# Optimization experiments

Hardware: AMD Instinct MI355X
Metric: run time of the kernel (lower is better)

## Reference

```python
import jax, jax.numpy as jnp
import numpy as np

DIM = 128
HEADS = 4
GH, GW = 14, 14
N = GH * GW            # 196
POS_DIM = (DIM // 4) // 4  # 8, per DynamicPosBias(dim//4): pos_dim = (dim//4)//4
B_ = 1024
NW = 64
EPS = 1e-5


def _make_bias_tables():
    # biases: all relative (dh, dw) offsets, shape ((2*GH-1)*(2*GW-1), 2)
    h = np.arange(1 - GH, GH)
    w = np.arange(1 - GW, GW)
    bh, bw = np.meshgrid(h, w, indexing='ij')
    biases = np.stack([bh.ravel(), bw.ravel()], axis=1).astype(np.float32)
    # relative_position_index: (N, N) int
    ch, cw = np.meshgrid(np.arange(GH), np.arange(GW), indexing='ij')
    coords = np.stack([ch.ravel(), cw.ravel()])          # (2, N)
    rel = coords[:, :, None] - coords[:, None, :]        # (2, N, N)
    rel = rel.transpose(1, 2, 0).copy()
    rel[:, :, 0] += GH - 1
    rel[:, :, 1] += GW - 1
    rel[:, :, 0] *= 2 * GW - 1
    idx = rel.sum(-1).astype(np.int32)                   # (N, N)
    return jnp.asarray(biases), jnp.asarray(idx)


def setup_inputs() -> dict:
    key = jax.random.key(0)
    ks = jax.random.split(key, 12)
    s_in = 1.0 / np.sqrt(DIM)
    s_p = 1.0 / np.sqrt(POS_DIM)
    biases, rel_idx = _make_bias_tables()
    return {
        'x': jax.random.normal(ks[0], (B_, N, DIM), jnp.float32),
        'mask': jnp.zeros((NW, N, N), jnp.float32),
        # qkv / proj (stored as (in, out), i.e. torch weight transposed)
        'qkv_w': jax.random.normal(ks[1], (DIM, 3 * DIM), jnp.float32) * s_in,
        'qkv_b': jnp.zeros((3 * DIM,), jnp.float32),
        'proj_w': jax.random.normal(ks[2], (DIM, DIM), jnp.float32) * s_in,
        'proj_b': jnp.zeros((DIM,), jnp.float32),
        # DynamicPosBias params
        'pos_proj_w': jax.random.normal(ks[3], (2, POS_DIM), jnp.float32) * 0.5,
        'pos_proj_b': jnp.zeros((POS_DIM,), jnp.float32),
        'ln1_w': jnp.ones((POS_DIM,), jnp.float32), 'ln1_b': jnp.zeros((POS_DIM,), jnp.float32),
        'fc1_w': jax.random.normal(ks[4], (POS_DIM, POS_DIM), jnp.float32) * s_p,
        'fc1_b': jnp.zeros((POS_DIM,), jnp.float32),
        'ln2_w': jnp.ones((POS_DIM,), jnp.float32), 'ln2_b': jnp.zeros((POS_DIM,), jnp.float32),
        'fc2_w': jax.random.normal(ks[5], (POS_DIM, POS_DIM), jnp.float32) * s_p,
        'fc2_b': jnp.zeros((POS_DIM,), jnp.float32),
        'ln3_w': jnp.ones((POS_DIM,), jnp.float32), 'ln3_b': jnp.zeros((POS_DIM,), jnp.float32),
        'fc3_w': jax.random.normal(ks[6], (POS_DIM, HEADS), jnp.float32) * s_p,
        'fc3_b': jnp.zeros((HEADS,), jnp.float32),
        'biases': biases,       # ((2GH-1)*(2GW-1), 2) float32
        'rel_idx': rel_idx,     # (N, N) int32
    }


def _ln(x, w, b):
    mu = x.mean(-1, keepdims=True)
    var = ((x - mu) ** 2).mean(-1, keepdims=True)
    return (x - mu) * jax.lax.rsqrt(var + EPS) * w + b


def reference(x, mask, qkv_w, qkv_b, proj_w, proj_b,
              pos_proj_w, pos_proj_b,
              ln1_w, ln1_b, fc1_w, fc1_b,
              ln2_w, ln2_b, fc2_w, fc2_b,
              ln3_w, ln3_b, fc3_w, fc3_b,
              biases, rel_idx):
    B, n, C = x.shape
    hd = C // HEADS
    scale = hd ** -0.5

    qkv = (x @ qkv_w + qkv_b).reshape(B, n, 3, HEADS, hd)
    q, k, v = jnp.moveaxis(qkv, 2, 0)          # each (B, n, H, hd)
    q = q * scale
    attn = jnp.einsum('bqhd,bkhd->bhqk', q, k)  # (B, H, n, n)

    # DynamicPosBias (residual=False): pos3(pos2(pos1(pos_proj(biases))))
    p = biases @ pos_proj_w + pos_proj_b
    p = jax.nn.relu(_ln(p, ln1_w, ln1_b)) @ fc1_w + fc1_b
    p = jax.nn.relu(_ln(p, ln2_w, ln2_b)) @ fc2_w + fc2_b
    p = jax.nn.relu(_ln(p, ln3_w, ln3_b)) @ fc3_w + fc3_b   # (L, H)
    rpb = p[rel_idx]                            # (n, n, H) gather
    attn = attn + jnp.transpose(rpb, (2, 0, 1))[None]

    nW = mask.shape[0]
    attn = attn.reshape(B // nW, nW, HEADS, n, n) + mask[None, :, None]
    attn = jax.nn.softmax(attn.reshape(B, HEADS, n, n), axis=-1)

    out = jnp.einsum('bhqk,bkhd->bqhd', attn, v).reshape(B, n, C)
    return out @ proj_w + proj_b
```

## Files before the change

### kernel.cpp

```cpp
#include <hip/hip_runtime.h>
#include <stdint.h>

#define N_TOK 196
#define DIM   128
#define HEADS 4
#define NWIN  64
#define SCALE 0.17677669529663687f
#define LOG2E 1.4426950408889634f
#define PS_LD 232

typedef __bf16 bf16x8 __attribute__((ext_vector_type(8)));
typedef float  f32x4  __attribute__((ext_vector_type(4)));

__device__ __forceinline__ unsigned short f2bf(float f) {
  unsigned r;
  asm("v_cvt_pk_bf16_f32 %0, %1, %2" : "=v"(r) : "v"(f), "v"(f));
  return (unsigned short)r;
}
__device__ __forceinline__ unsigned pack2(float a, float b) {
  unsigned r;
  asm("v_cvt_pk_bf16_f32 %0, %1, %2" : "=v"(r) : "v"(a), "v"(b));
  return r;
}
__device__ __forceinline__ float fexp2(float x) {
  float r;
  asm("v_exp_f32 %0, %1" : "=v"(r) : "v"(x));
  return r;
}

__global__ void prep_kernel(
    const float* __restrict__ qkv_w, const float* __restrict__ proj_w,
    const float* __restrict__ biases,
    const float* __restrict__ pos_proj_w, const float* __restrict__ pos_proj_b,
    const float* __restrict__ ln1_w, const float* __restrict__ ln1_b,
    const float* __restrict__ fc1_w, const float* __restrict__ fc1_b,
    const float* __restrict__ ln2_w, const float* __restrict__ ln2_b,
    const float* __restrict__ fc2_w, const float* __restrict__ fc2_b,
    const float* __restrict__ ln3_w, const float* __restrict__ ln3_b,
    const float* __restrict__ fc3_w, const float* __restrict__ fc3_b,
    unsigned short* __restrict__ wqkv_t, unsigned short* __restrict__ wproj_t,
    float* __restrict__ ptab)
{
  const int tid = threadIdx.x, blk = blockIdx.x;
  if (blk < 3) {
    int r = blk * 256 + tid;
    if (r < 729) {
      float v[8], t[8];
      float b0 = biases[2*r], b1 = biases[2*r+1];
      for (int j = 0; j < 8; ++j)
        v[j] = b0 * pos_proj_w[j] + b1 * pos_proj_w[8+j] + pos_proj_b[j];
      const float* lws[3] = {ln1_w, ln2_w, ln3_w};
      const float* lbs[3] = {ln1_b, ln2_b, ln3_b};
      const float* fws[3] = {fc1_w, fc2_w, fc3_w};
      const float* fbs[3] = {fc1_b, fc2_b, fc3_b};
      for (int L = 0; L < 3; ++L) {
        float mu = 0.f;  for (int j=0;j<8;++j) mu += v[j];  mu *= 0.125f;
        float var = 0.f; for (int j=0;j<8;++j){ float d=v[j]-mu; var+=d*d; } var *= 0.125f;
        float rs = rsqrtf(var + 1e-5f);
        for (int j=0;j<8;++j){ float u=(v[j]-mu)*rs*lws[L][j]+lbs[L][j]; t[j]=fmaxf(u,0.f); }
        int nout = (L==2) ? 4 : 8;
        for (int o=0;o<nout;++o){ float s=fbs[L][o]; for (int j=0;j<8;++j) s += t[j]*fws[L][j*nout+o]; v[o]=s; }
      }
      for (int hh=0; hh<4; ++hh) ptab[r*4+hh] = v[hh];
    }
  } else if (blk < 7) {
    for (int i = (blk-3)*256 + tid; i < 384*128; i += 1024) {
      int col = i >> 7, k = i & 127;
      wqkv_t[i] = f2bf(qkv_w[k*384 + col]);
    }
  } else {
    for (int i = tid; i < 128*128; i += 256) {
      int col = i >> 7, k = i & 127;
      wproj_t[i] = f2bf(proj_w[k*128 + col]);
    }
  }
}

__global__ void comb_kernel(const int* __restrict__ rel_idx,
                            const float* __restrict__ ptab,
                            const float* __restrict__ mask,
                            float* __restrict__ combT)
{
  int blk = blockIdx.x;
  int w = blk / 196, k = blk - w*196;
  int q = threadIdx.x;
  if (q < N_TOK) {
    int idx = rel_idx[q*N_TOK + k];
    float mv = mask[((size_t)w*N_TOK + q)*N_TOK + k];
    #pragma unroll
    for (int h = 0; h < 4; ++h)
      combT[((size_t)(w*4 + h)*196 + k)*196 + q] = (ptab[idx*4 + h] + mv) * LOG2E;
  }
}

__launch_bounds__(256, 2)
__global__ void qkv_kernel(const float* __restrict__ x,
                           const float* __restrict__ qkv_b,
                           const unsigned short* __restrict__ wqkv_t,
                           unsigned short* __restrict__ q_g,
                           unsigned short* __restrict__ k_g,
                           unsigned short* __restrict__ vt_g)
{
  const int tid = threadIdx.x;
  const int wave = tid >> 6, lane = tid & 63, lr = lane & 15, lg = lane >> 4;
  const int b = blockIdx.x;
  const float* xb = x + (size_t)b * (N_TOK*DIM);

  bf16x8 wf[6][4];
  float  bq[6];
  f32x4  bv[6];
  #pragma unroll
  for (int i = 0; i < 6; ++i) {
    const int g = wave*6 + i;
    #pragma unroll
    for (int kc = 0; kc < 4; ++kc)
      wf[i][kc] = *(const bf16x8*)(wqkv_t + (g*16 + lr)*128 + kc*32 + lg*8);
    if (g < 16) {
      bq[i] = qkv_b[g*16 + lr];
      bv[i] = (f32x4){0.f,0.f,0.f,0.f};
    } else {
      bq[i] = 0.f;
      #pragma unroll
      for (int r = 0; r < 4; ++r) bv[i][r] = qkv_b[g*16 + lg*4 + r];
    }
  }

  auto load_xf = [&](int rt, bf16x8* xf) {
    const int arow = rt*16 + lr;
    #pragma unroll
    for (int kc = 0; kc < 4; ++kc) {
      union { unsigned u[4]; bf16x8 v; } c;
      if (arow < N_TOK) {
        float4 p0 = *(const float4*)(xb + arow*DIM + kc*32 + lg*8);
        float4 p1 = *(const float4*)(xb + arow*DIM + kc*32 + lg*8 + 4);
        c.u[0] = pack2(p0.x, p0.y); c.u[1] = pack2(p0.z, p0.w);
        c.u[2] = pack2(p1.x, p1.y); c.u[3] = pack2(p1.z, p1.w);
      } else {
        c.u[0] = c.u[1] = c.u[2] = c.u[3] = 0u;
      }
      xf[kc] = c.v;
    }
  };

  bf16x8 xf[4], xfn[4];
  load_xf(0, xf);
  for (int rt = 0; rt < 13; ++rt) {
    if (rt < 12) load_xf(rt + 1, xfn);
    #pragma unroll
    for (int i = 0; i < 6; ++i) {
      const int g = wave*6 + i;
      f32x4 acc = {0.f,0.f,0.f,0.f};
      if (g >= 16) {
        #pragma unroll
        for (int kc = 0; kc < 4; ++kc)
          acc = __builtin_amdgcn_mfma_f32_16x16x32_bf16(wf[i][kc], xf[kc], acc, 0, 0, 0);
        const int dt = g - 16;
        #pragma unroll
        for (int r = 0; r < 4; ++r)
          vt_g[((size_t)b*128 + dt*16 + lg*4 + r)*224 + rt*16 + lr] =
              f2bf(acc[r] + bv[i][r]);
      } else {
        #pragma unroll
        for (int kc = 0; kc < 4; ++kc)
          acc = __builtin_amdgcn_mfma_f32_16x16x32_bf16(xf[kc], wf[i][kc], acc, 0, 0, 0);
        const int cs = (g < 8) ? g*16 : (g-8)*16;
        unsigned short* dst = (g < 8) ? q_g : k_g;
        const float mul = (g < 8) ? (SCALE * LOG2E) : 1.f;
        #pragma unroll
        for (int r = 0; r < 4; ++r)
          dst[((size_t)(b*4 + (cs>>5))*208 + rt*16 + lg*4 + r)*32 + (cs&31) + lr] =
              f2bf((acc[r] + bq[i]) * mul);
      }
    }
    #pragma unroll
    for (int kc = 0; kc < 4; ++kc) xf[kc] = xfn[kc];
  }
}

__launch_bounds__(256, 3)
__global__ void attn_kernel(const unsigned short* __restrict__ q_g,
                            const unsigned short* __restrict__ k_g,
                            const unsigned short* __restrict__ vt_g,
                            const float* __restrict__ combT,
                            float* __restrict__ out)
{
  __shared__ unsigned short psw_all[4*16*PS_LD];
  const int tid = threadIdx.x;
  const int wave = tid >> 6, lane = tid & 63, lr = lane & 15, lg = lane >> 4;
  const int wgt = blockIdx.x;
  const int v  = (wgt & 7)*512 + (wgt >> 3);
  const int bi = v & 15, wh = v >> 4;
  const int b  = bi*64 + (wh >> 2), h = wh & 3;
  const int bh = b*4 + h;
  unsigned short* psw = psw_all + wave*(16*PS_LD);

  for (int i = lane; i < 256; i += 64)
    psw[(i >> 4)*PS_LD + 208 + (i & 15)] = 0;

  const unsigned short* qb = q_g + (size_t)bh*(208*32);
  const unsigned short* kb = k_g + (size_t)bh*(208*32);
  const unsigned short* vb = vt_g + (size_t)bh*(32*224);
  const float* cbase = combT + (size_t)wh*(196*196);

  bf16x8 kfr[13];
  #pragma unroll
  for (int kt = 0; kt < 13; ++kt)
    kfr[kt] = *(const bf16x8*)(kb + (kt*16 + lr)*32 + lg*8);

  for (int qt = wave; qt < 13; qt += 4) {
    bf16x8 aq = *(const bf16x8*)(qb + (qt*16 + lr)*32 + lg*8);

    f32x4 s[13];
    #pragma unroll
    for (int kt = 0; kt < 13; ++kt) {
      int c = kt*16 + lr;
      s[kt] = (c < N_TOK) ? *(const f32x4*)(cbase + (size_t)c*196 + qt*16 + lg*4)
                          : (f32x4){0.f,0.f,0.f,0.f};
    }

    __builtin_amdgcn_s_setprio(1);
    #pragma unroll
    for (int kt = 0; kt < 13; ++kt)
      s[kt] = __builtin_amdgcn_mfma_f32_16x16x32_bf16(aq, kfr[kt], s[kt], 0, 0, 0);
    __builtin_amdgcn_s_setprio(0);

    #pragma unroll
    for (int kt = 0; kt < 13; ++kt) {
      #pragma unroll
      for (int r = 0; r < 4; ++r) s[kt][r] = fexp2(s[kt][r]);
    }
    if (lr >= 4) s[12] = (f32x4){0.f,0.f,0.f,0.f};

    float linv[4];
    #pragma unroll
    for (int r = 0; r < 4; ++r) {
      float ssum = 0.f;
      #pragma unroll
      for (int kt = 0; kt < 13; ++kt) ssum += s[kt][r];
      #pragma unroll
      for (int off = 1; off < 16; off <<= 1) ssum += __shfl_xor(ssum, off);
      linv[r] = 1.f / ssum;
    }

    #pragma unroll
    for (int r = 0; r < 4; ++r) {
      int prow = lg*4 + r;
      #pragma unroll
      for (int kt = 0; kt < 13; ++kt)
        psw[prow*PS_LD + kt*16 + lr] = f2bf(s[kt][r]);
    }
    asm volatile("s_waitcnt lgkmcnt(0)" ::: "memory");

    __builtin_amdgcn_s_setprio(1);
    #pragma unroll
    for (int c2 = 0; c2 < 2; ++c2) {
      f32x4 o = {0.f,0.f,0.f,0.f};
      #pragma unroll
      for (int kc = 0; kc < 7; ++kc) {
        bf16x8 ap = *(const bf16x8*)(psw + lr*PS_LD + kc*32 + lg*8);
        bf16x8 bv = *(const bf16x8*)(vb + (c2*16 + lr)*224 + kc*32 + lg*8);
        o = __builtin_amdgcn_mfma_f32_16x16x32_bf16(ap, bv, o, 0, 0, 0);
      }
      #pragma unroll
      for (int r = 0; r < 4; ++r) {
        int row = qt*16 + lg*4 + r;
        if (row < N_TOK)
          out[((size_t)b*N_TOK + row)*DIM + h*32 + c2*16 + lr] = o[r] * linv[r];
      }
    }
    __builtin_amdgcn_s_setprio(0);
  }
}

__launch_bounds__(256, 4)
__global__ void proj_kernel(float* __restrict__ out,
                            const unsigned short* __restrict__ wproj_t,
                            const float* __restrict__ proj_b)
{
  __shared__ unsigned short aos[64*136];
  const int tid = threadIdx.x;
  const int wave = tid >> 6, lane = tid & 63, lr = lane & 15, lg = lane >> 4;
  const size_t row0 = (size_t)blockIdx.x * 64;
  const float* src = out + row0*DIM;

  bf16x8 wf[2][4];
  float bias[2];
  #pragma unroll
  for (int i = 0; i < 2; ++i) {
    int ct = wave*2 + i;
    bias[i] = proj_b[ct*16 + lr];
    #pragma unroll
    for (int kc = 0; kc < 4; ++kc)
      wf[i][kc] = *(const bf16x8*)(wproj_t + (ct*16 + lr)*128 + kc*32 + lg*8);
  }

  for (int i = tid; i < 64*32; i += 256) {
    int lrow = i >> 5, c4 = i & 31;
    float4 v = ((const float4*)src)[i];
    ((uint2*)aos)[lrow*34 + c4] = make_uint2(pack2(v.x, v.y), pack2(v.z, v.w));
  }
  __syncthreads();

  for (int rt = 0; rt < 4; ++rt) {
    bf16x8 af[4];
    #pragma unroll
    for (int kc = 0; kc < 4; ++kc)
      af[kc] = *(const bf16x8*)(aos + (rt*16 + lr)*136 + kc*32 + lg*8);
    #pragma unroll
    for (int i = 0; i < 2; ++i) {
      f32x4 acc = {0.f,0.f,0.f,0.f};
      #pragma unroll
      for (int kc = 0; kc < 4; ++kc)
        acc = __builtin_amdgcn_mfma_f32_16x16x32_bf16(af[kc], wf[i][kc], acc, 0, 0, 0);
      #pragma unroll
      for (int r = 0; r < 4; ++r) {
        size_t grow = row0 + rt*16 + lg*4 + r;
        out[grow*DIM + (wave*2 + i)*16 + lr] = acc[r] + bias[i];
      }
    }
  }
}

extern "C" void kernel_launch(void* const* d_in, const int* in_sizes, int n_in,
                              void* d_out, int out_size, void* d_ws, size_t ws_size,
                              hipStream_t stream)
{
  const float* x          = (const float*)d_in[0];
  const float* mask       = (const float*)d_in[1];
  const float* qkv_w      = (const float*)d_in[2];
  const float* qkv_b      = (const float*)d_in[3];
  const float* proj_w     = (const float*)d_in[4];
  const float* proj_b     = (const float*)d_in[5];
  const float* pos_proj_w = (const float*)d_in[6];
  const float* pos_proj_b = (const float*)d_in[7];
  const float* ln1_w = (const float*)d_in[8];
  const float* ln1_b = (const float*)d_in[9];
  const float* fc1_w = (const float*)d_in[10];
  const float* fc1_b = (const float*)d_in[11];
  const float* ln2_w = (const float*)d_in[12];
  const float* ln2_b = (const float*)d_in[13];
  const float* fc2_w = (const float*)d_in[14];
  const float* fc2_b = (const float*)d_in[15];
  const float* ln3_w = (const float*)d_in[16];
  const float* ln3_b = (const float*)d_in[17];
  const float* fc3_w = (const float*)d_in[18];
  const float* fc3_b = (const float*)d_in[19];
  const float* biases = (const float*)d_in[20];
  const int*   rel_idx = (const int*)d_in[21];

  char* ws = (char*)d_ws;
  unsigned short* wqkv_t  = (unsigned short*)(ws);
  unsigned short* wproj_t = (unsigned short*)(ws + 98304);
  float*          ptab    = (float*)(ws + 131072);
  float*          combT   = (float*)(ws + 147456);
  unsigned short* q_g     = (unsigned short*)(ws + 39485696);
  unsigned short* k_g     = (unsigned short*)(ws + 94011648);
  unsigned short* vt_g    = (unsigned short*)(ws + 148537600);
  float* out = (float*)d_out;

  prep_kernel<<<8, 256, 0, stream>>>(qkv_w, proj_w, biases, pos_proj_w, pos_proj_b,
      ln1_w, ln1_b, fc1_w, fc1_b, ln2_w, ln2_b, fc2_w, fc2_b,
      ln3_w, ln3_b, fc3_w, fc3_b, wqkv_t, wproj_t, ptab);
  comb_kernel<<<NWIN*N_TOK, 256, 0, stream>>>(rel_idx, ptab, mask, combT);
  qkv_kernel<<<1024, 256, 0, stream>>>(x, qkv_b, wqkv_t, q_g, k_g, vt_g);
  attn_kernel<<<1024*HEADS, 256, 0, stream>>>(q_g, k_g, vt_g, combT, out);
  proj_kernel<<<(1024*N_TOK)/64, 256, 0, stream>>>(out, wproj_t, proj_b);
}
```

Before: 373.5 us.

## Store attention output as bf16 in q buffer and read it directly in proj

The attention kernel now writes its normalized output as bf16 into the q workspace slice it has already consumed, instead of writing fp32 into the final output buffer. The projection kernel then reads those bf16 fragments straight from global memory per head, so the fp32 round trip and the LDS staging pass with its barrier go away. The launch-bounds occupancy hint on the attention kernel is also raised from 3 to 5 blocks. In-place reuse of q depends on each wave finishing its q-tile read before writing the same rows, and the higher occupancy target may force register spills.

```diff
diff --git a/kernel.cpp b/kernel.cpp
--- a/kernel.cpp
+++ b/kernel.cpp
@@ -177,12 +177,11 @@
   }
 }
 
-__launch_bounds__(256, 3)
-__global__ void attn_kernel(const unsigned short* __restrict__ q_g,
+__launch_bounds__(256, 5)
+__global__ void attn_kernel(unsigned short* q_g,
                             const unsigned short* __restrict__ k_g,
                             const unsigned short* __restrict__ vt_g,
-                            const float* __restrict__ combT,
-                            float* __restrict__ out)
+                            const float* __restrict__ combT)
 {
   __shared__ unsigned short psw_all[4*16*PS_LD];
   const int tid = threadIdx.x;
@@ -197,7 +196,7 @@
   for (int i = lane; i < 256; i += 64)
     psw[(i >> 4)*PS_LD + 208 + (i & 15)] = 0;
 
-  const unsigned short* qb = q_g + (size_t)bh*(208*32);
+  unsigned short* qb = q_g + (size_t)bh*(208*32);
   const unsigned short* kb = k_g + (size_t)bh*(208*32);
   const unsigned short* vb = vt_g + (size_t)bh*(32*224);
   const float* cbase = combT + (size_t)wh*(196*196);
@@ -265,7 +264,7 @@
       for (int r = 0; r < 4; ++r) {
         int row = qt*16 + lg*4 + r;
         if (row < N_TOK)
-          out[((size_t)b*N_TOK + row)*DIM + h*32 + c2*16 + lr] = o[r] * linv[r];
+          qb[row*32 + c2*16 + lr] = f2bf(o[r] * linv[r]);
       }
     }
     __builtin_amdgcn_s_setprio(0);
@@ -273,15 +272,14 @@
 }
 
 __launch_bounds__(256, 4)
-__global__ void proj_kernel(float* __restrict__ out,
+__global__ void proj_kernel(const unsigned short* __restrict__ att,
                             const unsigned short* __restrict__ wproj_t,
-                            const float* __restrict__ proj_b)
-{
-  __shared__ unsigned short aos[64*136];
+                            const float* __restrict__ proj_b,
+                            float* __restrict__ out)
+{
   const int tid = threadIdx.x;
   const int wave = tid >> 6, lane = tid & 63, lr = lane & 15, lg = lane >> 4;
-  const size_t row0 = (size_t)blockIdx.x * 64;
-  const float* src = out + row0*DIM;
+  const int row0 = blockIdx.x * 64;
 
   bf16x8 wf[2][4];
   float bias[2];
@@ -294,18 +292,13 @@
       wf[i][kc] = *(const bf16x8*)(wproj_t + (ct*16 + lr)*128 + kc*32 + lg*8);
   }
 
-  for (int i = tid; i < 64*32; i += 256) {
-    int lrow = i >> 5, c4 = i & 31;
-    float4 v = ((const float4*)src)[i];
-    ((uint2*)aos)[lrow*34 + c4] = make_uint2(pack2(v.x, v.y), pack2(v.z, v.w));
-  }
-  __syncthreads();
-
   for (int rt = 0; rt < 4; ++rt) {
+    const int g = row0 + rt*16 + lr;
+    const int b = g / 196, tok = g - b*196;
     bf16x8 af[4];
     #pragma unroll
     for (int kc = 0; kc < 4; ++kc)
-      af[kc] = *(const bf16x8*)(aos + (rt*16 + lr)*136 + kc*32 + lg*8);
+      af[kc] = *(const bf16x8*)(att + ((size_t)(b*4 + kc)*208 + tok)*32 + lg*8);
     #pragma unroll
     for (int i = 0; i < 2; ++i) {
       f32x4 acc = {0.f,0.f,0.f,0.f};
@@ -313,10 +306,9 @@
       for (int kc = 0; kc < 4; ++kc)
         acc = __builtin_amdgcn_mfma_f32_16x16x32_bf16(af[kc], wf[i][kc], acc, 0, 0, 0);
       #pragma unroll
-      for (int r = 0; r < 4; ++r) {
-        size_t grow = row0 + rt*16 + lg*4 + r;
-        out[grow*DIM + (wave*2 + i)*16 + lr] = acc[r] + bias[i];
-      }
+      for (int r = 0; r < 4; ++r)
+        out[(size_t)(row0 + rt*16 + lg*4 + r)*DIM + (wave*2 + i)*16 + lr] =
+            acc[r] + bias[i];
     }
   }
 }
@@ -363,6 +355,6 @@
       ln3_w, ln3_b, fc3_w, fc3_b, wqkv_t, wproj_t, ptab);
   comb_kernel<<<NWIN*N_TOK, 256, 0, stream>>>(rel_idx, ptab, mask, combT);
   qkv_kernel<<<1024, 256, 0, stream>>>(x, qkv_b, wqkv_t, q_g, k_g, vt_g);
-  attn_kernel<<<1024*HEADS, 256, 0, stream>>>(q_g, k_g, vt_g, combT, out);
-  proj_kernel<<<(1024*N_TOK)/64, 256, 0, stream>>>(out, wproj_t, proj_b);
-}
+  attn_kernel<<<1024*HEADS, 256, 0, stream>>>(q_g, k_g, vt_g, combT);
+  proj_kernel<<<(1024*N_TOK)/64, 256, 0, stream>>>(q_g, wproj_t, proj_b, out);
+}
```

New measurement: 571.0 us. 52.9% more time.
